# Optimization experiments

Measured on AMD Instinct MI355X. Metric: run time of the kernel, lower is better.

Reference implementation:

```python
import jax, jax.numpy as jnp
import numpy as np

EPS = 1e-5
K = 2  # superpatch hop


def _bn(x, gamma, beta, mean, var):
    # inference-mode BatchNorm2d over channel dim (NCHW)
    inv = gamma / jnp.sqrt(var + EPS)
    return x * inv[None, :, None, None] + (beta - mean * inv)[None, :, None, None]


def _conv1x1(x, w, b):
    # x: [B,C,H,W], w: [O,C], b: [O]
    return jnp.einsum('bchw,oc->bohw', x, w) + b[None, :, None, None]


def setup_inputs() -> dict:
    key = jax.random.key(0)
    ks = jax.random.split(key, 24)
    B, C, H, W = 32, 192, 56, 56
    r = lambda k, shape, s=0.05: jax.random.normal(k, shape, dtype=jnp.float32) * s
    pv = lambda k, shape: jax.random.uniform(k, shape, dtype=jnp.float32, minval=0.5, maxval=1.5)
    inp = {
        'x': jax.random.normal(ks[0], (B, C, H, W), dtype=jnp.float32),
        # RepCPE: depthwise 7x7 conv, groups=C -> weight [C,1,7,7]
        'cpe_w': r(ks[1], (C, 1, 7, 7)),
        'cpe_b': r(ks[2], (C,)),
        # fc1: 1x1 conv C->C + BN
        'fc1_w': r(ks[3], (C, C)), 'fc1_b': r(ks[4], (C,)),
        'bn1_g': pv(ks[5], (C,)), 'bn1_b': r(ks[6], (C,)),
        'bn1_m': r(ks[7], (C,), 0.1), 'bn1_v': pv(ks[8], (C,)),
        # graph_conv.nn: 1x1 conv 2C->C + BN + GELU
        'gc_w': r(ks[9], (C, 2 * C)), 'gc_b': r(ks[10], (C,)),
        'bng_g': pv(ks[11], (C,)), 'bng_b': r(ks[12], (C,)),
        'bng_m': r(ks[13], (C,), 0.1), 'bng_v': pv(ks[14], (C,)),
        # fc2: 1x1 conv C->C + BN
        'fc2_w': r(ks[15], (C, C)), 'fc2_b': r(ks[16], (C,)),
        'bn2_g': pv(ks[17], (C,)), 'bn2_b': r(ks[18], (C,)),
        'bn2_m': r(ks[19], (C,), 0.1), 'bn2_v': pv(ks[20], (C,)),
    }
    return inp


def reference(x, cpe_w, cpe_b, fc1_w, fc1_b, bn1_g, bn1_b, bn1_m, bn1_v,
              gc_w, gc_b, bng_g, bng_b, bng_m, bng_v,
              fc2_w, fc2_b, bn2_g, bn2_b, bn2_m, bn2_v):
    C = x.shape[1]
    # --- RepCPE: depthwise 7x7 conv + bias, residual add ---
    pe = jax.lax.conv_general_dilated(
        x, cpe_w, window_strides=(1, 1), padding='SAME',
        feature_group_count=C,
        dimension_numbers=('NCHW', 'OIHW', 'NCHW'))
    x = pe + cpe_b[None, :, None, None] + x
    # --- fc1: 1x1 conv + BN ---
    x = _bn(_conv1x1(x, fc1_w, fc1_b), bn1_g, bn1_b, bn1_m, bn1_v)
    # --- MRConv4d: max-relative over 4 shifted neighbor views ---
    # torch.cat([x[..., -K:, :], x[..., :-K, :]], dim=2) == roll(+K) along H, etc.
    d = jnp.maximum(jnp.roll(x, K, axis=2) - x, jnp.roll(x, -K, axis=2) - x)
    d = jnp.maximum(d, jnp.roll(x, K, axis=3) - x)
    x_j = jnp.maximum(jnp.maximum(d, jnp.roll(x, -K, axis=3) - x), 0.0)  # x_j init = x - x = 0
    xc = jnp.concatenate([x, x_j], axis=1)  # [B,2C,H,W]
    x = jax.nn.gelu(_bn(_conv1x1(xc, gc_w, gc_b), bng_g, bng_b, bng_m, bng_v),
                    approximate=False)
    # --- fc2: 1x1 conv + BN ---
    x = _bn(_conv1x1(x, fc2_w, fc2_b), bn2_g, bn2_b, bn2_m, bn2_v)
    return x
```

## Files before the change

kernel.cpp:

```cpp
#include <hip/hip_runtime.h>
#include <hip/hip_bf16.h>
#include <hip/hip_fp16.h>


#define CC   192
#define HW   3136
#define NB   32
#define CP_STR 957

using short8 = __attribute__((ext_vector_type(8))) short;
using f32x4  = __attribute__((ext_vector_type(4))) float;

__device__ __forceinline__ float bf2f(short s) {
  union { unsigned u; float f; } x; x.u = ((unsigned)(unsigned short)s) << 16; return x.f;
}
__device__ __forceinline__ short f2bf(float f) {
  __hip_bfloat16 h = __float2bfloat16(f);
  return *reinterpret_cast<short*>(&h);
}
__device__ __forceinline__ unsigned pack_bf2(float a, float b) {
  return ((unsigned)(unsigned short)f2bf(a)) | (((unsigned)(unsigned short)f2bf(b)) << 16);
}
__device__ __forceinline__ unsigned pack_hf2(float a, float b) {
  __half2 h = __floats2half2_rn(a, b);
  union { __half2 h2; unsigned u; } c; c.h2 = h; return c.u;
}
__device__ __forceinline__ __half2 as_h2(unsigned u) {
  union { unsigned u; __half2 h2; } c; c.u = u; return c.h2;
}
__device__ __forceinline__ float geluf(float v) {
  float u = 0.7978845608028654f * (v + 0.044715f * v * v * v);
  float e = __expf(2.0f * u);
  return 0.5f * v * (2.0f - 2.0f / (e + 1.0f));
}
__device__ __forceinline__ void gl2lds(const char* g, char* l) {
  __builtin_amdgcn_global_load_lds(
      (const __attribute__((address_space(1))) void*)g,
      (__attribute__((address_space(3))) void*)l, 16, 0, 0);
}

__global__ void __launch_bounds__(256) fold_kernel(
    const float* __restrict__ fc1_w, const float* __restrict__ fc1_b,
    const float* __restrict__ bn1_g, const float* __restrict__ bn1_b,
    const float* __restrict__ bn1_m, const float* __restrict__ bn1_v,
    const float* __restrict__ gc_w,  const float* __restrict__ gc_b,
    const float* __restrict__ bng_g, const float* __restrict__ bng_b,
    const float* __restrict__ bng_m, const float* __restrict__ bng_v,
    const float* __restrict__ fc2_w, const float* __restrict__ fc2_b,
    const float* __restrict__ bn2_g, const float* __restrict__ bn2_b,
    const float* __restrict__ bn2_m, const float* __restrict__ bn2_v,
    __hip_bfloat16* __restrict__ W1f, __hip_bfloat16* __restrict__ Wgf, __hip_bfloat16* __restrict__ W2f,
    float* __restrict__ b1f, float* __restrict__ bgf, float* __restrict__ b2f) {
  int gt = blockIdx.x * 256 + threadIdx.x;
  if (gt < 3 * CC) {
    int which = gt / CC, o = gt - which * CC;
    const float *G, *Bt, *M, *V, *Bi; float* dst;
    if (which == 0)      { G = bn1_g; Bt = bn1_b; M = bn1_m; V = bn1_v; Bi = fc1_b; dst = b1f; }
    else if (which == 1) { G = bng_g; Bt = bng_b; M = bng_m; V = bng_v; Bi = gc_b;  dst = bgf; }
    else                 { G = bn2_g; Bt = bn2_b; M = bn2_m; V = bn2_v; Bi = fc2_b; dst = b2f; }
    float inv = G[o] * rsqrtf(V[o] + 1e-5f);
    dst[o] = Bi[o] * inv + Bt[o] - M[o] * inv;
  }
  int i = gt;
  if (i < CC * CC) {
    int o = i / CC;
    float inv = bn1_g[o] * rsqrtf(bn1_v[o] + 1e-5f);
    W1f[i] = __float2bfloat16(fc1_w[i] * inv);
  } else if (i < CC * CC + CC * 2 * CC) {
    int j = i - CC * CC; int o = j / (2 * CC);
    float inv = bng_g[o] * rsqrtf(bng_v[o] + 1e-5f);
    Wgf[j] = __float2bfloat16(gc_w[j] * inv);
  } else if (i < CC * CC * 4) {
    int j = i - CC * CC * 3; int o = j / CC;
    float inv = bn2_g[o] * rsqrtf(bn2_v[o] + 1e-5f);
    W2f[j] = __float2bfloat16(fc2_w[j] * inv);
  }
}

__global__ void __launch_bounds__(256, 4) dwconv_kernel(
    const float* __restrict__ x, const float* __restrict__ cw,
    const float* __restrict__ cb, __hip_bfloat16* __restrict__ y0pm) {
  __shared__ unsigned in_t2[8 * CP_STR];
  const int t = threadIdx.x;
  int bb = blockIdx.x;
  const int rs = bb % 7;  bb /= 7;
  const int cg = bb % 12; bb /= 12;
  const int b  = bb;
  const int h0 = rs * 8;

  for (int i = t; i < 8 * CP_STR / 4; i += 256) ((uint4*)in_t2)[i] = uint4{0, 0, 0, 0};
  __syncthreads();

  for (int it = t; it < 8 * 14 * 14; it += 256) {
    int w4 = it % 14, rr = (it / 14) % 14, cp = it / 196;
    int gh = h0 - 3 + rr;
    if (gh >= 0 && gh < 56) {
      const float* pa = x + ((size_t)(b * CC + cg * 16 + cp * 2) * 56 + gh) * 56 + w4 * 4;
      float4 va = *(const float4*)pa;
      float4 vb = *(const float4*)(pa + 3136);
      uint4 u;
      u.x = pack_hf2(va.x, vb.x); u.y = pack_hf2(va.y, vb.y);
      u.z = pack_hf2(va.z, vb.z); u.w = pack_hf2(va.w, vb.w);
      *(uint4*)(in_t2 + cp * CP_STR + rr * 68 + 4 + w4 * 4) = u;
    }
  }
  __syncthreads();

  const int cp = t & 7, g = t >> 3;
  const int cgx = g % 7, rq = g / 7;
  if (g < 28) {
    const float* wpA = cw + (cg * 16 + cp * 2) * 49;
    float biasA = cb[cg * 16 + cp * 2];
    float biasB = cb[cg * 16 + cp * 2 + 1];
    const unsigned* base = in_t2 + cp * CP_STR + rq * 2 * 68 + cgx * 8;
    __half2 acc2[2][8];
    const __half2 hz = __floats2half2_rn(0.0f, 0.0f);
#pragma unroll
    for (int r = 0; r < 2; ++r)
#pragma unroll
      for (int ww = 0; ww < 8; ++ww) acc2[r][ww] = hz;

    __half2 wr2[7], wn2[7];
#pragma unroll
    for (int i = 0; i < 7; ++i) wr2[i] = __floats2half2_rn(wpA[i], wpA[49 + i]);
#pragma unroll
    for (int kh = 0; kh < 7; ++kh) {
      if (kh < 6) {
#pragma unroll
        for (int i = 0; i < 7; ++i)
          wn2[i] = __floats2half2_rn(wpA[(kh + 1) * 7 + i], wpA[49 + (kh + 1) * 7 + i]);
      }
      if (kh == 3)
        wr2[3] = __floats2half2_rn(wpA[24] + 1.0f, wpA[73] + 1.0f);
#pragma unroll
      for (int r = 0; r < 2; ++r) {
        const unsigned* rp = base + (r + kh) * 68;
        uint4 d0 = *(const uint4*)(rp);
        uint4 d1 = *(const uint4*)(rp + 4);
        uint4 d2 = *(const uint4*)(rp + 8);
        uint4 d3 = *(const uint4*)(rp + 12);
        __half2 v2[16] = { as_h2(d0.x), as_h2(d0.y), as_h2(d0.z), as_h2(d0.w),
                           as_h2(d1.x), as_h2(d1.y), as_h2(d1.z), as_h2(d1.w),
                           as_h2(d2.x), as_h2(d2.y), as_h2(d2.z), as_h2(d2.w),
                           as_h2(d3.x), as_h2(d3.y), as_h2(d3.z), as_h2(d3.w) };
#pragma unroll
        for (int kw = 0; kw < 7; ++kw) {
#pragma unroll
          for (int ww = 0; ww < 8; ++ww)
            acc2[r][ww] = __hfma2(wr2[kw], v2[ww + kw + 1], acc2[r][ww]);
        }
      }
#pragma unroll
      for (int i = 0; i < 7; ++i) wr2[i] = wn2[i];
    }
    short* dst0 = (short*)y0pm + ((size_t)b * HW + (size_t)(h0 + rq * 2) * 56 + cgx * 8) * CC
                  + cg * 16 + cp * 2;
#pragma unroll
    for (int r = 0; r < 2; ++r)
#pragma unroll
      for (int ww = 0; ww < 8; ++ww) {
        float2 f = __half22float2(acc2[r][ww]);
        unsigned pv = pack_bf2(f.x + biasA, f.y + biasB);
        *(unsigned*)(dst0 + (size_t)(r * 56 + ww) * CC) = pv;
      }
  }
}

__device__ __forceinline__ void xj_load(short8 (&nb)[5], const short* y1c, int hwl) {
  int h = hwl / 56, w = hwl - h * 56;
  int hp = (h >= 54) ? h - 54 : h + 2;
  int hm = (h < 2) ? h + 54 : h - 2;
  int wp = (w >= 54) ? w - 54 : w + 2;
  int wm = (w < 2) ? w + 54 : w - 2;
  nb[0] = *(const short8*)(y1c + (size_t)hwl * CC);
  nb[1] = *(const short8*)(y1c + (size_t)(hp * 56 + w) * CC);
  nb[2] = *(const short8*)(y1c + (size_t)(hm * 56 + w) * CC);
  nb[3] = *(const short8*)(y1c + (size_t)(h * 56 + wp) * CC);
  nb[4] = *(const short8*)(y1c + (size_t)(h * 56 + wm) * CC);
}
__device__ __forceinline__ void xj_write(char* dst, const short8 (&nb)[5], int dstoff) {
  short8 res;
#pragma unroll
  for (int q = 0; q < 8; ++q) {
    float m = fmaxf(fmaxf(bf2f(nb[1][q]), bf2f(nb[2][q])),
                    fmaxf(bf2f(nb[3][q]), bf2f(nb[4][q])));
    res[q] = f2bf(fmaxf(m - bf2f(nb[0][q]), 0.0f));
  }
  *(short8*)(dst + dstoff) = res;
}

template<int MODE>
__global__ void __launch_bounds__(256, 2) gemm_kernel(
    const __hip_bfloat16* __restrict__ actA,
    const __hip_bfloat16* __restrict__ Wf, const float* __restrict__ bfv,
    void* __restrict__ outp) {
  __shared__ char smem[2][24576];
  const int t = threadIdx.x;
  const int lane = t & 63, w = t >> 6;
  const int lrow = lane & 15, lhi = lane >> 4;
  constexpr int NT = NB * 49;

  int goff[6];
#pragma unroll
  for (int j = 0; j < 6; ++j) {
    int idx = j * 4096 + t * 16;
    int p = idx / 384, qd = idx - p * 384;
    goff[j] = p * 384 + (qd ^ ((p & 7) << 4));
  }

  float bw0[3];
  float bw2[3][4];
  if (MODE != 2) {
#pragma unroll
    for (int wi = 0; wi < 3; ++wi) bw0[wi] = bfv[w * 48 + wi * 16 + lrow];
  } else {
#pragma unroll
    for (int wi = 0; wi < 3; ++wi)
#pragma unroll
      for (int r = 0; r < 4; ++r) bw2[wi][r] = bfv[w * 48 + wi * 16 + lhi * 4 + r];
  }

  short8 wreg[6][3];
#pragma unroll
  for (int kk = 0; kk < 6; ++kk)
#pragma unroll
    for (int wi = 0; wi < 3; ++wi) {
      int o = w * 48 + wi * 16 + lrow;
      wreg[kk][wi] = *(const short8*)((const short*)Wf + (size_t)o * 192 + kk * 32 + lhi * 8);
    }

  const int step = gridDim.x;
  int tile = blockIdx.x;
  {
    const char* src = (const char*)actA + (size_t)tile * 24576;
#pragma unroll
    for (int j = 0; j < 6; ++j)
      gl2lds(src + goff[j], smem[0] + j * 4096 + w * 1024);
  }
  __syncthreads();
  int cur = 0;

  while (tile < NT) {
    const int tnext = tile + step;
    f32x4 acc[4][3] = {};
    if (tnext < NT) {
      const char* nsrc = (const char*)actA + (size_t)tnext * 24576;
#pragma unroll
      for (int j = 0; j < 6; ++j)
        gl2lds(nsrc + goff[j], smem[cur ^ 1] + j * 4096 + w * 1024);
    }
#pragma unroll
    for (int kk = 0; kk < 6; ++kk) {
      short8 af[4];
#pragma unroll
      for (int ai = 0; ai < 4; ++ai) {
        int p = ai * 16 + lrow;
        af[ai] = *(const short8*)(smem[cur] + p * 384 + ((kk * 64 + lhi * 16) ^ ((p & 7) << 4)));
      }
#pragma unroll
      for (int ai = 0; ai < 4; ++ai)
#pragma unroll
        for (int wi = 0; wi < 3; ++wi)
          acc[ai][wi] = (MODE == 2)
              ? __builtin_amdgcn_mfma_f32_16x16x32_bf16(wreg[kk][wi], af[ai], acc[ai][wi], 0, 0, 0)
              : __builtin_amdgcn_mfma_f32_16x16x32_bf16(af[ai], wreg[kk][wi], acc[ai][wi], 0, 0, 0);
    }
    __syncthreads();
    cur ^= 1;

    if (MODE != 2) {
      short* ob = (short*)outp + (size_t)tile * 64 * CC;
#pragma unroll
      for (int wi = 0; wi < 3; ++wi) {
        int o = w * 48 + wi * 16 + lrow;
#pragma unroll
        for (int ai = 0; ai < 4; ++ai)
#pragma unroll
          for (int r = 0; r < 4; ++r) {
            int p = ai * 16 + lhi * 4 + r;
            ob[(size_t)p * CC + o] = f2bf(acc[ai][wi][r] + bw0[wi]);
          }
      }
    } else {
      int bimg = tile / 49, hwbase = (tile - bimg * 49) * 64;
      float* ob = (float*)outp + (size_t)bimg * CC * HW + hwbase;
#pragma unroll
      for (int wi = 0; wi < 3; ++wi)
#pragma unroll
        for (int r = 0; r < 4; ++r) {
          int o = w * 48 + wi * 16 + lhi * 4 + r;
#pragma unroll
          for (int ai = 0; ai < 4; ++ai)
            ob[(size_t)o * HW + ai * 16 + lrow] = acc[ai][wi][r] + bw2[wi][r];
        }
    }
    tile = tnext;
  }
}

__global__ void __launch_bounds__(768, 3) gemm2_kernel(
    const __hip_bfloat16* __restrict__ y1g, const __hip_bfloat16* __restrict__ Wf,
    const float* __restrict__ bfv, __hip_bfloat16* __restrict__ outp) {
  __shared__ char smem[2][24576];
  const int t = threadIdx.x;
  const int lane = t & 63, w = t >> 6;
  const int lrow = lane & 15, lhi = lane >> 4;
  constexpr int NT = NB * 49;

  int sp[2], sq[2], goff[2];
#pragma unroll
  for (int j = 0; j < 2; ++j) {
    int idx = j * 12288 + t * 16;
    sp[j] = idx / 384;
    sq[j] = idx - sp[j] * 384;
    goff[j] = sp[j] * 384 + (sq[j] ^ ((sp[j] & 7) << 4));
  }

  const float bw = bfv[w * 16 + lrow];

  short8 wreg[2][6];
#pragma unroll
  for (int c = 0; c < 2; ++c)
#pragma unroll
    for (int kk = 0; kk < 6; ++kk) {
      int o = w * 16 + lrow;
      wreg[c][kk] = *(const short8*)((const short*)Wf +
          (size_t)o * 384 + c * 192 + kk * 32 + lhi * 8);
    }

  const int step = gridDim.x;
  int tile = blockIdx.x;
  {
    const char* src = (const char*)y1g + (size_t)tile * 24576;
#pragma unroll
    for (int j = 0; j < 2; ++j)
      gl2lds(src + goff[j], smem[0] + j * 12288 + w * 1024);
  }
  __syncthreads();
  int cur = 0;

  while (tile < NT) {
    const int tnext = tile + step;
    const int bimg = tile / 49;
    const int hwbase = (tile - bimg * 49) * 64;
    const short* y1b = (const short*)y1g + (size_t)bimg * HW * CC;
    f32x4 acc[4] = {};

    short8 nbA[5], nbB[5];
    xj_load(nbA, y1b + (sq[0] >> 1), hwbase + sp[0]);
    xj_load(nbB, y1b + (sq[1] >> 1), hwbase + sp[1]);
#pragma unroll
    for (int kk = 0; kk < 6; ++kk) {
      short8 af[4];
#pragma unroll
      for (int ai = 0; ai < 4; ++ai) {
        int p = ai * 16 + lrow;
        af[ai] = *(const short8*)(smem[cur] + p * 384 + ((kk * 64 + lhi * 16) ^ ((p & 7) << 4)));
      }
#pragma unroll
      for (int ai = 0; ai < 4; ++ai)
        acc[ai] = __builtin_amdgcn_mfma_f32_16x16x32_bf16(af[ai], wreg[0][kk], acc[ai], 0, 0, 0);
    }
    xj_write(smem[cur ^ 1], nbA, goff[0]);
    xj_write(smem[cur ^ 1], nbB, goff[1]);
    __syncthreads();
    cur ^= 1;

    if (tnext < NT) {
      const char* nsrc = (const char*)y1g + (size_t)tnext * 24576;
#pragma unroll
      for (int j = 0; j < 2; ++j)
        gl2lds(nsrc + goff[j], smem[cur ^ 1] + j * 12288 + w * 1024);
    }
#pragma unroll
    for (int kk = 0; kk < 6; ++kk) {
      short8 af[4];
#pragma unroll
      for (int ai = 0; ai < 4; ++ai) {
        int p = ai * 16 + lrow;
        af[ai] = *(const short8*)(smem[cur] + p * 384 + ((kk * 64 + lhi * 16) ^ ((p & 7) << 4)));
      }
#pragma unroll
      for (int ai = 0; ai < 4; ++ai)
        acc[ai] = __builtin_amdgcn_mfma_f32_16x16x32_bf16(af[ai], wreg[1][kk], acc[ai], 0, 0, 0);
    }
    __syncthreads();
    cur ^= 1;

    short* ob = (short*)outp + (size_t)tile * 64 * CC;
    const int o = w * 16 + lrow;
#pragma unroll
    for (int ai = 0; ai < 4; ++ai)
#pragma unroll
      for (int r = 0; r < 4; ++r) {
        int p = ai * 16 + lhi * 4 + r;
        ob[(size_t)p * CC + o] = f2bf(geluf(acc[ai][r] + bw));
      }
    tile = tnext;
  }
}

extern "C" void kernel_launch(void* const* d_in, const int* in_sizes, int n_in,
                              void* d_out, int out_size, void* d_ws, size_t ws_size,
                              hipStream_t stream) {
  const float* x     = (const float*)d_in[0];
  const float* cpe_w = (const float*)d_in[1];
  const float* cpe_b = (const float*)d_in[2];
  const float* fc1_w = (const float*)d_in[3];
  const float* fc1_b = (const float*)d_in[4];
  const float* bn1_g = (const float*)d_in[5];
  const float* bn1_b = (const float*)d_in[6];
  const float* bn1_m = (const float*)d_in[7];
  const float* bn1_v = (const float*)d_in[8];
  const float* gc_w  = (const float*)d_in[9];
  const float* gc_b  = (const float*)d_in[10];
  const float* bng_g = (const float*)d_in[11];
  const float* bng_b = (const float*)d_in[12];
  const float* bng_m = (const float*)d_in[13];
  const float* bng_v = (const float*)d_in[14];
  const float* fc2_w = (const float*)d_in[15];
  const float* fc2_b = (const float*)d_in[16];
  const float* bn2_g = (const float*)d_in[17];
  const float* bn2_b = (const float*)d_in[18];
  const float* bn2_m = (const float*)d_in[19];
  const float* bn2_v = (const float*)d_in[20];

  if (ws_size < 77594624) return;
  char* ws = (char*)d_ws;
  __hip_bfloat16* W1f = (__hip_bfloat16*)(ws);
  __hip_bfloat16* Wgf = (__hip_bfloat16*)(ws + 73728);
  __hip_bfloat16* W2f = (__hip_bfloat16*)(ws + 221184);
  float* b1f = (float*)(ws + 294912);
  float* bgf = (float*)(ws + 295680);
  float* b2f = (float*)(ws + 296448);
  __hip_bfloat16* y0  = (__hip_bfloat16*)(ws + 524288);
  __hip_bfloat16* y1  = (__hip_bfloat16*)d_out;
  float* out = (float*)d_out;

  fold_kernel<<<576, 256, 0, stream>>>(fc1_w, fc1_b, bn1_g, bn1_b, bn1_m, bn1_v,
      gc_w, gc_b, bng_g, bng_b, bng_m, bng_v, fc2_w, fc2_b, bn2_g, bn2_b, bn2_m, bn2_v,
      W1f, Wgf, W2f, b1f, bgf, b2f);
  dwconv_kernel<<<NB * 12 * 7, 256, 0, stream>>>(x, cpe_w, cpe_b, y0);
  gemm_kernel<0><<<512, 256, 0, stream>>>(y0, W1f, b1f, y1);
  gemm2_kernel<<<512, 768, 0, stream>>>(y1, Wgf, bgf, y0);
  gemm_kernel<2><<<512, 256, 0, stream>>>(y0, W2f, b2f, out);
}
```

Measured before the change: 139.4 us.

## Fuse graph-conv GEMM and fc2 GEMM into one kernel via LDS staging

Merges the gelu graph-conv GEMM and the fc2 GEMM into a single kernel. The gelu output tile goes into LDS instead of a global bf16 buffer and is consumed directly by the fc2 MFMA loop. This removes one kernel launch and a full write and read of the intermediate activation. In exchange it uses three LDS buffers, drops the occupancy hint to one block per CU, and moves y1 into workspace because the output buffer is now written in the same kernel that reads y1.

```diff
diff --git a/kernel.cpp b/kernel.cpp
--- a/kernel.cpp
+++ b/kernel.cpp
@@ -209,16 +209,8 @@
   }
 
   float bw0[3];
-  float bw2[3][4];
-  if (MODE != 2) {
-#pragma unroll
-    for (int wi = 0; wi < 3; ++wi) bw0[wi] = bfv[w * 48 + wi * 16 + lrow];
-  } else {
-#pragma unroll
-    for (int wi = 0; wi < 3; ++wi)
-#pragma unroll
-      for (int r = 0; r < 4; ++r) bw2[wi][r] = bfv[w * 48 + wi * 16 + lhi * 4 + r];
-  }
+#pragma unroll
+  for (int wi = 0; wi < 3; ++wi) bw0[wi] = bfv[w * 48 + wi * 16 + lrow];
 
   short8 wreg[6][3];
 #pragma unroll
@@ -261,47 +253,32 @@
       for (int ai = 0; ai < 4; ++ai)
 #pragma unroll
         for (int wi = 0; wi < 3; ++wi)
-          acc[ai][wi] = (MODE == 2)
-              ? __builtin_amdgcn_mfma_f32_16x16x32_bf16(wreg[kk][wi], af[ai], acc[ai][wi], 0, 0, 0)
-              : __builtin_amdgcn_mfma_f32_16x16x32_bf16(af[ai], wreg[kk][wi], acc[ai][wi], 0, 0, 0);
+          acc[ai][wi] = __builtin_amdgcn_mfma_f32_16x16x32_bf16(af[ai], wreg[kk][wi], acc[ai][wi], 0, 0, 0);
     }
     __syncthreads();
     cur ^= 1;
 
-    if (MODE != 2) {
-      short* ob = (short*)outp + (size_t)tile * 64 * CC;
-#pragma unroll
-      for (int wi = 0; wi < 3; ++wi) {
-        int o = w * 48 + wi * 16 + lrow;
-#pragma unroll
-        for (int ai = 0; ai < 4; ++ai)
-#pragma unroll
-          for (int r = 0; r < 4; ++r) {
-            int p = ai * 16 + lhi * 4 + r;
-            ob[(size_t)p * CC + o] = f2bf(acc[ai][wi][r] + bw0[wi]);
-          }
-      }
-    } else {
-      int bimg = tile / 49, hwbase = (tile - bimg * 49) * 64;
-      float* ob = (float*)outp + (size_t)bimg * CC * HW + hwbase;
-#pragma unroll
-      for (int wi = 0; wi < 3; ++wi)
+    short* ob = (short*)outp + (size_t)tile * 64 * CC;
+#pragma unroll
+    for (int wi = 0; wi < 3; ++wi) {
+      int o = w * 48 + wi * 16 + lrow;
+#pragma unroll
+      for (int ai = 0; ai < 4; ++ai)
 #pragma unroll
         for (int r = 0; r < 4; ++r) {
-          int o = w * 48 + wi * 16 + lhi * 4 + r;
-#pragma unroll
-          for (int ai = 0; ai < 4; ++ai)
-            ob[(size_t)o * HW + ai * 16 + lrow] = acc[ai][wi][r] + bw2[wi][r];
+          int p = ai * 16 + lhi * 4 + r;
+          ob[(size_t)p * CC + o] = f2bf(acc[ai][wi][r] + bw0[wi]);
         }
     }
     tile = tnext;
   }
 }
 
-__global__ void __launch_bounds__(768, 3) gemm2_kernel(
-    const __hip_bfloat16* __restrict__ y1g, const __hip_bfloat16* __restrict__ Wf,
-    const float* __restrict__ bfv, __hip_bfloat16* __restrict__ outp) {
-  __shared__ char smem[2][24576];
+__global__ void __launch_bounds__(768, 1) gemm23_kernel(
+    const __hip_bfloat16* __restrict__ y1g, const __hip_bfloat16* __restrict__ Wgf,
+    const float* __restrict__ bgf, const __hip_bfloat16* __restrict__ W2f,
+    const float* __restrict__ b2f, float* __restrict__ outp) {
+  __shared__ char smem[3][24576];
   const int t = threadIdx.x;
   const int lane = t & 63, w = t >> 6;
   const int lrow = lane & 15, lhi = lane >> 4;
@@ -316,28 +293,39 @@
     goff[j] = sp[j] * 384 + (sq[j] ^ ((sp[j] & 7) << 4));
   }
 
-  const float bw = bfv[w * 16 + lrow];
-
-  short8 wreg[2][6];
+  const float bwg = bgf[w * 16 + lrow];
+  float bw2[4];
+#pragma unroll
+  for (int r = 0; r < 4; ++r) bw2[r] = b2f[w * 16 + lhi * 4 + r];
+
+  short8 wregG[2][6];
 #pragma unroll
   for (int c = 0; c < 2; ++c)
 #pragma unroll
     for (int kk = 0; kk < 6; ++kk) {
       int o = w * 16 + lrow;
-      wreg[c][kk] = *(const short8*)((const short*)Wf +
+      wregG[c][kk] = *(const short8*)((const short*)Wgf +
           (size_t)o * 384 + c * 192 + kk * 32 + lhi * 8);
     }
+  short8 wreg2[6];
+#pragma unroll
+  for (int kk = 0; kk < 6; ++kk) {
+    int o = w * 16 + lrow;
+    wreg2[kk] = *(const short8*)((const short*)W2f + (size_t)o * 192 + kk * 32 + lhi * 8);
+  }
 
   const int step = gridDim.x;
   int tile = blockIdx.x;
+  int a = 0, c = 2;
   {
     const char* src = (const char*)y1g + (size_t)tile * 24576;
 #pragma unroll
     for (int j = 0; j < 2; ++j)
-      gl2lds(src + goff[j], smem[0] + j * 12288 + w * 1024);
+      gl2lds(src + goff[j], smem[a] + j * 12288 + w * 1024);
   }
   __syncthreads();
-  int cur = 0;
+
+  const int o2 = (w * 16 + lrow) * 2;
 
   while (tile < NT) {
     const int tnext = tile + step;
@@ -355,22 +343,21 @@
 #pragma unroll
       for (int ai = 0; ai < 4; ++ai) {
         int p = ai * 16 + lrow;
-        af[ai] = *(const short8*)(smem[cur] + p * 384 + ((kk * 64 + lhi * 16) ^ ((p & 7) << 4)));
-      }
-#pragma unroll
-      for (int ai = 0; ai < 4; ++ai)
-        acc[ai] = __builtin_amdgcn_mfma_f32_16x16x32_bf16(af[ai], wreg[0][kk], acc[ai], 0, 0, 0);
-    }
-    xj_write(smem[cur ^ 1], nbA, goff[0]);
-    xj_write(smem[cur ^ 1], nbB, goff[1]);
+        af[ai] = *(const short8*)(smem[a] + p * 384 + ((kk * 64 + lhi * 16) ^ ((p & 7) << 4)));
+      }
+#pragma unroll
+      for (int ai = 0; ai < 4; ++ai)
+        acc[ai] = __builtin_amdgcn_mfma_f32_16x16x32_bf16(af[ai], wregG[0][kk], acc[ai], 0, 0, 0);
+    }
+    xj_write(smem[1], nbA, goff[0]);
+    xj_write(smem[1], nbB, goff[1]);
     __syncthreads();
-    cur ^= 1;
 
     if (tnext < NT) {
       const char* nsrc = (const char*)y1g + (size_t)tnext * 24576;
 #pragma unroll
       for (int j = 0; j < 2; ++j)
-        gl2lds(nsrc + goff[j], smem[cur ^ 1] + j * 12288 + w * 1024);
+        gl2lds(nsrc + goff[j], smem[c] + j * 12288 + w * 1024);
     }
 #pragma unroll
     for (int kk = 0; kk < 6; ++kk) {
@@ -378,24 +365,43 @@
 #pragma unroll
       for (int ai = 0; ai < 4; ++ai) {
         int p = ai * 16 + lrow;
-        af[ai] = *(const short8*)(smem[cur] + p * 384 + ((kk * 64 + lhi * 16) ^ ((p & 7) << 4)));
-      }
-#pragma unroll
-      for (int ai = 0; ai < 4; ++ai)
-        acc[ai] = __builtin_amdgcn_mfma_f32_16x16x32_bf16(af[ai], wreg[1][kk], acc[ai], 0, 0, 0);
-    }
-    __syncthreads();
-    cur ^= 1;
-
-    short* ob = (short*)outp + (size_t)tile * 64 * CC;
-    const int o = w * 16 + lrow;
+        af[ai] = *(const short8*)(smem[1] + p * 384 + ((kk * 64 + lhi * 16) ^ ((p & 7) << 4)));
+      }
+#pragma unroll
+      for (int ai = 0; ai < 4; ++ai)
+        acc[ai] = __builtin_amdgcn_mfma_f32_16x16x32_bf16(af[ai], wregG[1][kk], acc[ai], 0, 0, 0);
+    }
 #pragma unroll
     for (int ai = 0; ai < 4; ++ai)
 #pragma unroll
       for (int r = 0; r < 4; ++r) {
         int p = ai * 16 + lhi * 4 + r;
-        ob[(size_t)p * CC + o] = f2bf(geluf(acc[ai][r] + bw));
-      }
+        *(short*)(smem[a] + p * 384 + (o2 ^ ((p & 7) << 4))) = f2bf(geluf(acc[ai][r] + bwg));
+      }
+    __syncthreads();
+
+    f32x4 acc3[4] = {};
+#pragma unroll
+    for (int kk = 0; kk < 6; ++kk) {
+      short8 af[4];
+#pragma unroll
+      for (int ai = 0; ai < 4; ++ai) {
+        int p = ai * 16 + lrow;
+        af[ai] = *(const short8*)(smem[a] + p * 384 + ((kk * 64 + lhi * 16) ^ ((p & 7) << 4)));
+      }
+#pragma unroll
+      for (int ai = 0; ai < 4; ++ai)
+        acc3[ai] = __builtin_amdgcn_mfma_f32_16x16x32_bf16(wreg2[kk], af[ai], acc3[ai], 0, 0, 0);
+    }
+    float* ob = outp + (size_t)bimg * CC * HW + hwbase;
+#pragma unroll
+    for (int r = 0; r < 4; ++r) {
+      int o = w * 16 + lhi * 4 + r;
+#pragma unroll
+      for (int ai = 0; ai < 4; ++ai)
+        ob[(size_t)o * HW + ai * 16 + lrow] = acc3[ai][r] + bw2[r];
+    }
+    int tmp = a; a = c; c = tmp;
     tile = tnext;
   }
 }
@@ -434,7 +440,7 @@
   float* bgf = (float*)(ws + 295680);
   float* b2f = (float*)(ws + 296448);
   __hip_bfloat16* y0  = (__hip_bfloat16*)(ws + 524288);
-  __hip_bfloat16* y1  = (__hip_bfloat16*)d_out;
+  __hip_bfloat16* y1  = (__hip_bfloat16*)(ws + 39059456);
   float* out = (float*)d_out;
 
   fold_kernel<<<576, 256, 0, stream>>>(fc1_w, fc1_b, bn1_g, bn1_b, bn1_m, bn1_v,
@@ -442,6 +448,5 @@
       W1f, Wgf, W2f, b1f, bgf, b2f);
   dwconv_kernel<<<NB * 12 * 7, 256, 0, stream>>>(x, cpe_w, cpe_b, y0);
   gemm_kernel<0><<<512, 256, 0, stream>>>(y0, W1f, b1f, y1);
-  gemm2_kernel<<<512, 768, 0, stream>>>(y1, Wgf, bgf, y0);
-  gemm_kernel<2><<<512, 256, 0, stream>>>(y0, W2f, b2f, out);
-}
+  gemm23_kernel<<<512, 768, 0, stream>>>(y1, Wgf, bgf, W2f, b2f, out);
+}
```

New measurement: 162.5 us. +16.6%, slower.
